# Performance work log

Measured on AMD Instinct MI355X. Metric: run time of the kernel, lower is better.

Reference implementation:

```python
import jax, jax.numpy as jnp
import numpy as np

NUM_FEATURE = 512
HIDDEN = 256
NUM_CLASSES = 10
L1 = 1e-4
ALPHA = 1e-3
BATCH = 65536


def setup_inputs() -> dict:
    key = jax.random.key(0)
    k = jax.random.split(key, 6)
    x = jax.random.normal(k[0], (BATCH, NUM_FEATURE), dtype=jnp.float32)
    y = jax.random.randint(k[1], (BATCH,), 0, NUM_CLASSES, dtype=jnp.int32)
    fc0 = jax.random.normal(k[2], (NUM_FEATURE, 512), dtype=jnp.float32) / NUM_FEATURE
    fc1 = jax.random.normal(k[3], (NUM_FEATURE, 512), dtype=jnp.float32) / NUM_FEATURE
    w = jax.random.normal(k[4], (NUM_FEATURE, HIDDEN), dtype=jnp.float32) / NUM_FEATURE
    w1 = jax.random.normal(k[5], (HIDDEN, NUM_CLASSES), dtype=jnp.float32) / HIDDEN
    return {"x": x, "y": y, "fc0": fc0, "fc1": fc1, "w": w, "w1": w1}


def reference(x, y, fc0, fc1, w, w1):
    # sigmoid-gated MLP block with residual
    x1 = x @ fc0                                   # [B, 512]
    x2 = jax.nn.relu(x @ fc1)                      # [B, 512]
    x4 = x + (1.0 + jax.nn.sigmoid(x1)) * x2       # [B, 512] residual

    # head (Dropout(p=0.0) is identity)
    logits = jax.nn.relu(x4 @ w) @ w1              # [B, 10]
    pred = jnp.argmax(logits, axis=1)

    # cross-entropy (mean over batch)
    logp = jax.nn.log_softmax(logits, axis=-1)
    ce = -jnp.mean(jnp.take_along_axis(logp, y[:, None].astype(jnp.int32), axis=1))

    # L1 penalty on all weight matrices
    l1_pen = L1 * (jnp.abs(w1).sum() + jnp.abs(w).sum()
                   + jnp.abs(fc0).sum() + jnp.abs(fc1).sum())

    # per-class variance: sum_i ||mean_{y_i} - x4_i||^2, vectorized via segment sums
    counts = jax.ops.segment_sum(jnp.ones((x4.shape[0],), jnp.float32), y,
                                 num_segments=NUM_CLASSES)
    sums = jax.ops.segment_sum(x4, y, num_segments=NUM_CLASSES)   # [10, 512]
    means = sums / jnp.maximum(counts, 1.0)[:, None]
    var_loss = jnp.sum(jnp.square(means[y] - x4))

    loss = ce + l1_pen + ALPHA * var_loss
    acc = jnp.mean((pred.astype(jnp.int32) == y.astype(jnp.int32)).astype(jnp.float32))
    return (loss, acc)
```

## Files before the change

kernel.cpp:

```cpp
#include <hip/hip_runtime.h>
#include <stdint.h>

#define BATCH 65536
#define FDIM 512
#define HDIM 256
#define NC 10
#define NREP 16

typedef short short8 __attribute__((ext_vector_type(8)));
typedef float f32x4 __attribute__((ext_vector_type(4)));

#define OFF_FC0T   ((size_t)0)
#define OFF_FC1T   (OFF_FC0T + (size_t)512*512*2)
#define OFF_WT     (OFF_FC1T + (size_t)512*512*2)
#define OFF_XT     (OFF_WT   + (size_t)256*512*2)
#define OFF_X4T    (OFF_XT   + (size_t)BATCH*512*2)
#define OFF_ACC    (OFF_X4T  + (size_t)BATCH*512*2)
#define SCAL_SUMSQ 0
#define SCAL_CE    16
#define SCAL_ACC   32
#define SCAL_L1    48
#define SCAL_N     128
#define CNT_OFF    SCAL_N
#define GSUM_OFF   (SCAL_N + NREP*16)
#define ACC_FLOATS (GSUM_OFF + NREP*5120)
#define OFF_W1T    (OFF_ACC + (size_t)ACC_FLOATS*4)

#define GLL(g,l) __builtin_amdgcn_global_load_lds((const __attribute__((address_space(1))) void*)(g), (__attribute__((address_space(3))) void*)(l), 16, 0, 0)

__device__ __forceinline__ unsigned short f2b(float f){
  unsigned u = __float_as_uint(f);
  u += 0x7FFFu + ((u >> 16) & 1u);
  return (unsigned short)(u >> 16);
}
__device__ __forceinline__ float b2f(unsigned short h){
  return __uint_as_float(((unsigned)h) << 16);
}
__device__ __forceinline__ unsigned pk2b(float f0, float f1){
  unsigned u0 = __float_as_uint(f0) + 0x8000u;
  unsigned u1 = __float_as_uint(f1) + 0x8000u;
  return __builtin_amdgcn_perm(u1, u0, 0x07060302u);
}

__global__ __launch_bounds__(256) void k_setup(
    const float* __restrict__ x,   const float* __restrict__ fc0,
    const float* __restrict__ fc1, const float* __restrict__ w,
    const float* __restrict__ w1,
    unsigned short* __restrict__ xT,   unsigned short* __restrict__ fc0T,
    unsigned short* __restrict__ fc1T, unsigned short* __restrict__ wT,
    unsigned short* __restrict__ w1T,  float* __restrict__ accb)
{
  int blk = blockIdx.x, t = threadIdx.x;
  if (blk < 1024){
    int I = blk*4 + (t >> 6);
    int l = t & 63;
    int row = I*16 + (l & 15), q = l >> 4;
    const float* src = x + (size_t)row*FDIM + q*8;
    #pragma unroll
    for (int C = 0; C < 16; ++C){
      float4 v0 = *(const float4*)(src + C*32);
      float4 v1 = *(const float4*)(src + C*32 + 4);
      unsigned o[4];
      o[0] = pk2b(v0.x, v0.y); o[1] = pk2b(v0.z, v0.w);
      o[2] = pk2b(v1.x, v1.y); o[3] = pk2b(v1.z, v1.w);
      *(short8*)&xT[(((size_t)I*16 + C) << 9) + l*8] = *(short8*)o;
    }
    return;
  }
  if (blk < 1360){
    int i = (blk - 1024)*256 + t;
    float l1v = 0.f;
    if (i < 32768){
      int n4 = i&15, m = (i>>4)&3, C = (i>>6)&15, J = i>>10;
      int n = J*16+n4, k8 = C*4+m;
      unsigned short o[8];
      #pragma unroll
      for (int j=0;j<8;++j){ float v = fc0[(size_t)(k8*8+j)*512 + n]; o[j]=f2b(v); l1v += fabsf(v); }
      *(short8*)&fc0T[(size_t)(J*16+C)*512 + (i&63)*8] = *(short8*)o;
    } else if (i < 65536){
      int j0 = i - 32768;
      int n4 = j0&15, m = (j0>>4)&3, C = (j0>>6)&15, J = j0>>10;
      int n = J*16+n4, k8 = C*4+m;
      unsigned short o[8];
      #pragma unroll
      for (int j=0;j<8;++j){ float v = fc1[(size_t)(k8*8+j)*512 + n]; o[j]=f2b(v); l1v += fabsf(v); }
      *(short8*)&fc1T[(size_t)(J*16+C)*512 + (j0&63)*8] = *(short8*)o;
    } else if (i < 81920){
      int j0 = i - 65536;
      int n4 = j0&15, m = (j0>>4)&3, C = (j0>>6)&15, J = j0>>10;
      int n = J*16+n4, k8 = C*4+m;
      unsigned short o[8];
      #pragma unroll
      for (int j=0;j<8;++j){ float v = w[(size_t)(k8*8+j)*256 + n]; o[j]=f2b(v); l1v += fabsf(v); }
      *(short8*)&wT[(size_t)(J*16+C)*512 + (j0&63)*8] = *(short8*)o;
    } else if (i < 86016){
      int j0 = i - 81920;
      int C = j0 >> 9, l = (j0 >> 3) & 63, e = j0 & 7;
      int n = l & 15, k = C*32 + (l>>4)*8 + e;
      float v = (n < NC) ? w1[k*NC + n] : 0.f;
      w1T[C*512 + l*8 + e] = f2b(v);
      if (n < NC) l1v = fabsf(v);
    }
    for (int off = 32; off; off >>= 1) l1v += __shfl_down(l1v, off);
    if ((t & 63) == 0 && l1v != 0.f)
      atomicAdd(&accb[SCAL_L1 + (blk & (NREP-1))], l1v);
    return;
  }
  {
    int base = (blk - 1360)*1024;
    #pragma unroll
    for (int j=0;j<4;++j){
      int idx = base + j*256 + t;
      if (idx < ACC_FLOATS) accb[idx] = 0.f;
    }
  }
}

__global__ __launch_bounds__(256) void k_gemm12(
    const unsigned short* __restrict__ xT,
    const unsigned short* __restrict__ fc0T,
    const unsigned short* __restrict__ fc1T,
    unsigned short* __restrict__ x4T,
    float* __restrict__ scal)
{
  __shared__ __align__(16) char lds[32768];
  unsigned short* As    = (unsigned short*)lds;
  unsigned short* Bs0   = (unsigned short*)(lds + 16384);
  unsigned short* Bs1   = (unsigned short*)(lds + 24576);
  unsigned short* trans = (unsigned short*)(lds + 16384);
  __shared__ float red[4];

  int blk = blockIdx.x;
  int xcd = blk & 7, s = blk >> 3;
  int rowblk = xcd*64 + (s >> 3);
  int colblk = s & 7;

  int t = threadIdx.x;
  int wv = t >> 6, lane = t & 63, ln = lane & 15, quad = lane >> 4;
  int wr = wv >> 1, wc = wv & 1;

  const f32x4 zv = {0.f,0.f,0.f,0.f};
  f32x4 acc1[4][2], acc2[4][2];
  #pragma unroll
  for (int rt=0;rt<4;++rt){ acc1[rt][0]=zv; acc1[rt][1]=zv; acc2[rt][0]=zv; acc2[rt][1]=zv; }

  const char* xb  = (const char*)xT;
  const char* b0b = (const char*)fc0T;
  const char* b1b = (const char*)fc1T;

  for (int kt = 0; kt < 8; ++kt){
    #pragma unroll
    for (int i = 0; i < 2; ++i)
      #pragma unroll
      for (int c = 0; c < 2; ++c){
        size_t Ig = (size_t)(rowblk*8 + wv*2 + i);
        GLL(xb + ((Ig*16 + kt*2 + c) << 10) + lane*16,
            (char*)As + (((wv*2+i)*2 + c) << 10));
      }
    {
      size_t Jg = (size_t)(colblk*4 + wv);
      const char* g0 = b0b + ((Jg*16 + kt*2) << 10) + lane*16;
      const char* g1 = b1b + ((Jg*16 + kt*2) << 10) + lane*16;
      GLL(g0,        (char*)Bs0 + ((wv*2+0) << 10));
      GLL(g0 + 1024, (char*)Bs0 + ((wv*2+1) << 10));
      GLL(g1,        (char*)Bs1 + ((wv*2+0) << 10));
      GLL(g1 + 1024, (char*)Bs1 + ((wv*2+1) << 10));
    }
    __syncthreads();
    #pragma unroll
    for (int c = 0; c < 2; ++c){
      short8 a[4];
      #pragma unroll
      for (int rt=0;rt<4;++rt)
        a[rt] = *(const short8*)&As[(((wr*4+rt)*2 + c) << 9) + lane*8];
      #pragma unroll
      for (int ct=0;ct<2;++ct){
        int jl = wc*2 + ct;
        short8 b0 = *(const short8*)&Bs0[((jl*2+c) << 9) + lane*8];
        #pragma unroll
        for (int rt=0;rt<4;++rt)
          acc1[rt][ct] = __builtin_amdgcn_mfma_f32_16x16x32_bf16(a[rt], b0, acc1[rt][ct], 0,0,0);
        short8 b1 = *(const short8*)&Bs1[((jl*2+c) << 9) + lane*8];
        #pragma unroll
        for (int rt=0;rt<4;++rt)
          acc2[rt][ct] = __builtin_amdgcn_mfma_f32_16x16x32_bf16(a[rt], b1, acc2[rt][ct], 0,0,0);
      }
    }
    __syncthreads();
  }

  #pragma unroll
  for (int i = 0; i < 2; ++i)
    #pragma unroll
    for (int c = 0; c < 2; ++c){
      size_t Ig = (size_t)(rowblk*8 + wv*2 + i);
      GLL(xb + ((Ig*16 + colblk*2 + c) << 10) + lane*16,
          (char*)As + (((wv*2+i)*2 + c) << 10));
    }
  __syncthreads();

  float sumsq = 0.f;
  #pragma unroll
  for (int rt=0;rt<4;++rt){
    #pragma unroll
    for (int ct=0;ct<2;++ct){
      int slot_hi = (ct*2 + (ln>>3)) << 4;
      int elem = ln & 7;
      #pragma unroll
      for (int r=0;r<4;++r){
        int addr = (((wr*4+rt)*2 + wc) << 9) + ((quad*4+r) | slot_hi)*8 + elem;
        float xv  = b2f(As[addr]);
        float x1v = acc1[rt][ct][r];
        float x2v = fmaxf(acc2[rt][ct][r], 0.f);
        float gate = 1.f + 1.f/(1.f + __expf(-x1v));
        float x4v = fmaf(gate, x2v, xv);
        unsigned short ub = f2b(x4v);
        float fq = b2f(ub);
        sumsq = fmaf(fq, fq, sumsq);
        trans[addr] = ub;
      }
    }
  }
  for (int off = 32; off; off >>= 1) sumsq += __shfl_down(sumsq, off);
  if (lane == 0) red[wv] = sumsq;
  __syncthreads();
  if (t == 0)
    atomicAdd(&scal[SCAL_SUMSQ + (blk & (NREP-1))], red[0]+red[1]+red[2]+red[3]);
  {
    int lt = t >> 4;
    int I_local = lt >> 1, C_local = lt & 1;
    size_t gbase = ((size_t)(rowblk*8 + I_local)*16 + colblk*2 + C_local) << 9;
    int s0 = (t & 15)*32;
    #pragma unroll
    for (int j=0;j<4;++j)
      *(short8*)&x4T[gbase + s0 + j*8] = *(const short8*)&trans[(lt << 9) + s0 + j*8];
  }
}

__global__ __launch_bounds__(256) void k_csum(const unsigned short* __restrict__ x4T,
                                              const int* __restrict__ y,
                                              float* __restrict__ gsum){
  int w = blockIdx.x*4 + (threadIdx.x >> 6);
  int l = threadIdx.x & 63;
  int C = w & 15, Ig = w >> 4;
  int rl = l & 15, q = l >> 4;
  float a[NC][8];
  #pragma unroll
  for (int c=0;c<NC;++c)
    #pragma unroll
    for (int e=0;e<8;++e) a[c][e]=0.f;
  for (int ii = 0; ii < 64; ++ii){
    int I = Ig*64 + ii;
    int yv = y[I*16 + rl];
    short8 v = *(const short8*)&x4T[(((size_t)I*16 + C) << 9) + l*8];
    float f[8];
    #pragma unroll
    for (int e=0;e<8;++e) f[e] = b2f((unsigned short)v[e]);
    #pragma unroll
    for (int c=0;c<NC;++c){
      bool m = (yv == c);
      #pragma unroll
      for (int e=0;e<8;++e) a[c][e] += m ? f[e] : 0.f;
    }
  }
  #pragma unroll
  for (int off = 1; off < 16; off <<= 1)
    #pragma unroll
    for (int c=0;c<NC;++c)
      #pragma unroll
      for (int e=0;e<8;++e) a[c][e] += __shfl_xor(a[c][e], off);
  if (rl == 0){
    int rep = Ig & (NREP-1);
    int kb = C*32 + q*8;
    #pragma unroll
    for (int c=0;c<NC;++c)
      #pragma unroll
      for (int e=0;e<8;++e)
        atomicAdd(&gsum[(size_t)rep*5120 + c*512 + kb + e], a[c][e]);
  }
}

__global__ __launch_bounds__(256) void k_cnt(const int* __restrict__ y,
                                             float* __restrict__ gcnt){
  __shared__ float cntS[NC];
  int t = threadIdx.x;
  if (t < NC) cntS[t] = 0.f;
  __syncthreads();
  int base = blockIdx.x*2048;
  for (int i = t; i < 2048; i += 256) atomicAdd(&cntS[y[base+i]], 1.f);
  __syncthreads();
  if (t < NC) atomicAdd(&gcnt[(blockIdx.x & (NREP-1))*16 + t], cntS[t]);
}

__global__ __launch_bounds__(512) void k_gemm3_head(
    const unsigned short* __restrict__ x4T,
    const unsigned short* __restrict__ wT,
    const unsigned short* __restrict__ w1T,
    const int* __restrict__ y,
    float* __restrict__ scal)
{
  __shared__ __align__(16) char lds[49152];
  unsigned short* As     = (unsigned short*)lds;
  unsigned short* Bs     = (unsigned short*)(lds + 16384);
  unsigned short* transH = (unsigned short*)lds;
  __shared__ __align__(16) unsigned short w1s[4096];
  __shared__ float redc[8], reda[8];

  int blk = blockIdx.x;
  int t = threadIdx.x;
  int wv = t >> 6, lane = t & 63, ln = lane & 15, quad = lane >> 4;
  int wr = wv >> 2, wc = wv & 3;
  int rep = (blk ^ (blk >> 4)) & (NREP-1);

  *(short8*)&w1s[t*8] = *(const short8*)&w1T[t*8];

  const f32x4 zv = {0.f,0.f,0.f,0.f};
  f32x4 acc[4][4];
  #pragma unroll
  for (int rt=0;rt<4;++rt)
    #pragma unroll
    for (int ct=0;ct<4;++ct) acc[rt][ct] = zv;

  const char* ab = (const char*)x4T;
  const char* bb = (const char*)wT;

  for (int kt = 0; kt < 8; ++kt){
    {
      size_t Ig = (size_t)(blk*8 + wv);
      GLL(ab + ((Ig*16 + kt*2 + 0) << 10) + lane*16, (char*)As + ((wv*2+0) << 10));
      GLL(ab + ((Ig*16 + kt*2 + 1) << 10) + lane*16, (char*)As + ((wv*2+1) << 10));
    }
    #pragma unroll
    for (int i = 0; i < 2; ++i)
      #pragma unroll
      for (int c = 0; c < 2; ++c){
        size_t Jg = (size_t)(wv*2 + i);
        GLL(bb + ((Jg*16 + kt*2 + c) << 10) + lane*16,
            (char*)Bs + (((wv*2+i)*2 + c) << 10));
      }
    __syncthreads();
    #pragma unroll
    for (int c = 0; c < 2; ++c){
      short8 a[4];
      #pragma unroll
      for (int rt=0;rt<4;++rt)
        a[rt] = *(const short8*)&As[(((wr*4+rt)*2 + c) << 9) + lane*8];
      #pragma unroll
      for (int ct=0;ct<4;++ct){
        short8 b = *(const short8*)&Bs[(((wc*4+ct)*2 + c) << 9) + lane*8];
        #pragma unroll
        for (int rt=0;rt<4;++rt)
          acc[rt][ct] = __builtin_amdgcn_mfma_f32_16x16x32_bf16(a[rt], b, acc[rt][ct], 0,0,0);
      }
    }
    __syncthreads();
  }

  f32x4 alog = zv;
  #pragma unroll
  for (int hf = 0; hf < 2; ++hf){
    __syncthreads();
    if ((wc >> 1) == hf){
      #pragma unroll
      for (int rt=0;rt<4;++rt)
        #pragma unroll
        for (int ct=0;ct<4;++ct)
          #pragma unroll
          for (int r=0;r<4;++r){
            int row_l = wr*64 + rt*16 + quad*4 + r;
            int ch = (wc & 1)*64 + ct*16 + ln;
            int tile = ((row_l >> 4) << 2) | (ch >> 5);
            int slot = (row_l & 15) | (((ch >> 3) & 3) << 4);
            transH[(tile << 9) + slot*8 + (ch & 7)] = f2b(fmaxf(acc[rt][ct][r], 0.f));
          }
    }
    __syncthreads();
    #pragma unroll
    for (int Cl = 0; Cl < 4; ++Cl){
      short8 a = *(const short8*)&transH[((wv*4 + Cl) << 9) + lane*8];
      short8 b = *(const short8*)&w1s[(hf*4 + Cl)*512 + lane*8];
      alog = __builtin_amdgcn_mfma_f32_16x16x32_bf16(a, b, alog, 0,0,0);
    }
  }

  float ce_l = 0.f, acc_l = 0.f;
  #pragma unroll
  for (int r = 0; r < 4; ++r){
    int grow = blk*128 + wv*16 + quad*4 + r;
    int yv = y[grow];
    float lg = (ln < NC) ? alog[r] : -1e30f;
    float m = lg; int mi = ln;
    #pragma unroll
    for (int mk = 1; mk < 16; mk <<= 1){
      float om = __shfl_xor(m, mk); int oi = __shfl_xor(mi, mk);
      if (om > m || (om == m && oi < mi)){ m = om; mi = oi; }
    }
    float e  = (ln < NC) ? __expf(lg - m) : 0.f;
    float sy = (ln == yv) ? lg : 0.f;
    #pragma unroll
    for (int mk = 1; mk < 16; mk <<= 1){ e += __shfl_xor(e, mk); sy += __shfl_xor(sy, mk); }
    float lse = m + __logf(e);
    if (ln == 0){ ce_l += (lse - sy); acc_l += (mi == yv) ? 1.f : 0.f; }
  }
  ce_l  += __shfl_down(ce_l, 16);  acc_l += __shfl_down(acc_l, 16);
  ce_l  += __shfl_down(ce_l, 32);  acc_l += __shfl_down(acc_l, 32);
  if (lane == 0){ redc[wv] = ce_l; reda[wv] = acc_l; }
  __syncthreads();
  if (t == 0){
    float c = 0.f, a = 0.f;
    #pragma unroll
    for (int i=0;i<8;++i){ c += redc[i]; a += reda[i]; }
    atomicAdd(&scal[SCAL_CE  + rep], c);
    atomicAdd(&scal[SCAL_ACC + rep], a);
  }
}

__global__ __launch_bounds__(1024) void k_final(const float* __restrict__ accb,
                                                float* __restrict__ out){
  const float* gsum = accb + GSUM_OFF;
  const float* gcnt = accb + CNT_OFF;
  int t = threadIdx.x;
  float contrib = 0.f;
  for (int idx = t; idx < 5120; idx += 1024){
    float S = 0.f;
    #pragma unroll
    for (int r = 0; r < NREP; ++r) S += gsum[(size_t)r*5120 + idx];
    int c = idx >> 9;
    float cnt = 0.f;
    #pragma unroll
    for (int r = 0; r < NREP; ++r) cnt += gcnt[r*16 + c];
    contrib += S*S / fmaxf(cnt, 1.f);
  }
  for (int off = 32; off; off >>= 1) contrib += __shfl_down(contrib, off);
  __shared__ float red[16];
  if ((t & 63) == 0) red[t >> 6] = contrib;
  __syncthreads();
  if (t == 0){
    float var2 = 0.f;
    #pragma unroll
    for (int i=0;i<16;++i) var2 += red[i];
    float sumsq=0.f, ce=0.f, acc=0.f, l1=0.f;
    for (int r=0;r<NREP;++r){
      sumsq += accb[SCAL_SUMSQ+r];
      ce    += accb[SCAL_CE+r];
      acc   += accb[SCAL_ACC+r];
      l1    += accb[SCAL_L1+r];
    }
    float var_loss = sumsq - var2;
    out[0] = ce/(float)BATCH + 1e-4f*l1 + 1e-3f*var_loss;
    out[1] = acc/(float)BATCH;
  }
}

extern "C" void kernel_launch(void* const* d_in, const int* in_sizes, int n_in,
                              void* d_out, int out_size, void* d_ws, size_t ws_size,
                              hipStream_t stream){
  (void)in_sizes; (void)n_in; (void)out_size; (void)ws_size;
  const float* x   = (const float*)d_in[0];
  const int*   y   = (const int*)d_in[1];
  const float* fc0 = (const float*)d_in[2];
  const float* fc1 = (const float*)d_in[3];
  const float* w   = (const float*)d_in[4];
  const float* w1  = (const float*)d_in[5];
  char* ws = (char*)d_ws;
  unsigned short* fc0T = (unsigned short*)(ws + OFF_FC0T);
  unsigned short* fc1T = (unsigned short*)(ws + OFF_FC1T);
  unsigned short* wT   = (unsigned short*)(ws + OFF_WT);
  unsigned short* xT   = (unsigned short*)(ws + OFF_XT);
  unsigned short* x4T  = (unsigned short*)(ws + OFF_X4T);
  unsigned short* w1T  = (unsigned short*)(ws + OFF_W1T);
  float* accb = (float*)(ws + OFF_ACC);
  float* scal = accb;
  float* gcnt = accb + CNT_OFF;
  float* gsum = accb + GSUM_OFF;

  k_setup<<<1441, 256, 0, stream>>>(x, fc0, fc1, w, w1, xT, fc0T, fc1T, wT, w1T, accb);
  k_gemm12<<<4096, 256, 0, stream>>>(xT, fc0T, fc1T, x4T, scal);
  k_cnt<<<32, 256, 0, stream>>>(y, gcnt);
  k_csum<<<256, 256, 0, stream>>>(x4T, y, gsum);
  k_gemm3_head<<<512, 512, 0, stream>>>(x4T, wT, w1T, y, scal);
  k_final<<<1, 1024, 0, stream>>>(accb, (float*)d_out);
}
```

Baseline: 410.1 us.

## Restructure gate GEMM into 256x128 tiles with double-buffered LDS pipeline

Rewrites the fused fc0/fc1 GEMM kernel to use 512-thread blocks computing 256-row by 128-column tiles, with 128 KB of dynamic LDS split into two buffers. Global-to-LDS loads for the next K steps are interleaved with MFMA phases under explicit barriers, vmcnt waits and raised priority around the MFMA phases. Larger tiles cut redundant reloads of x and the weights, and the prefetching is meant to hide load latency behind compute. The cost is more registers per thread and heavy LDS use, which limits how many blocks fit on each CU.

Result: no change. 404.5 us (-1.4%).

```diff
diff --git a/kernel.cpp b/kernel.cpp
--- a/kernel.cpp
+++ b/kernel.cpp
@@ -116,124 +116,172 @@
   }
 }
 
-__global__ __launch_bounds__(256) void k_gemm12(
+
+#define BARRIER() __builtin_amdgcn_s_barrier()
+#define LGKM0() do{ asm volatile("s_waitcnt lgkmcnt(0)" ::: "memory"); \
+                    __builtin_amdgcn_sched_barrier(0); }while(0)
+
+#define READA(A, AB, H) do{                                                   \
+  _Pragma("unroll") for (int c_=0;c_<2;++c_)                                  \
+  _Pragma("unroll") for (int m_=0;m_<4;++m_)                                  \
+    A[c_][m_] = *(const short8*)((AB) + (((wr*8 + (H)*4 + m_)*2 + c_)<<10) + lane*16); \
+}while(0)
+
+#define READB(B, BB, MAT) do{                                                 \
+  _Pragma("unroll") for (int c_=0;c_<2;++c_)                                  \
+  _Pragma("unroll") for (int n_=0;n_<2;++n_)                                  \
+    B[c_][n_] = *(const short8*)((BB) + (MAT)*16384 + (((wc*2+n_)*2 + c_)<<10) + lane*16); \
+}while(0)
+
+#define MM(ACC, MB, A, B) do{                                                 \
+  __builtin_amdgcn_s_setprio(1);                                              \
+  _Pragma("unroll") for (int c_=0;c_<2;++c_)                                  \
+  _Pragma("unroll") for (int n_=0;n_<2;++n_)                                  \
+  _Pragma("unroll") for (int m_=0;m_<4;++m_)                                  \
+    ACC[(MB)+m_][n_] = __builtin_amdgcn_mfma_f32_16x16x32_bf16(A[c_][m_], B[c_][n_], ACC[(MB)+m_][n_], 0,0,0); \
+  __builtin_amdgcn_s_setprio(0);                                              \
+}while(0)
+
+#define STAGEA(KT2, H) do{                                                    \
+  char* d_ = ldsd + (((KT2)&1) ? 65536 : 0);                                  \
+  _Pragma("unroll") for (int r_=0;r_<2;++r_){                                 \
+    int idx_ = r_*8 + wv, q_ = idx_>>1, C_ = idx_&1;                          \
+    int Il_ = (q_&3) + ((q_>>2)<<3) + (H)*4;                                  \
+    GLL(xb + (((size_t)((rowblk*16 + Il_)*16 + (KT2)*2 + C_)) << 10) + lane*16, \
+        d_ + ((Il_*2 + C_) << 10) + lane*16);                                 \
+  } }while(0)
+
+#define STAGEB(KT2, MAT) do{                                                  \
+  char* d_ = ldsd + (((KT2)&1) ? 65536 : 0) + 32768 + (MAT)*16384;            \
+  const char* s_ = (MAT) ? b1b : b0b;                                         \
+  _Pragma("unroll") for (int r_=0;r_<2;++r_){                                 \
+    int idx_ = r_*8 + wv, J_ = idx_>>1, C_ = idx_&1;                          \
+    GLL(s_ + (((size_t)((colblk*8 + J_)*16 + (KT2)*2 + C_)) << 10) + lane*16, \
+        d_ + ((J_*2 + C_) << 10) + lane*16);                                  \
+  } }while(0)
+
+__global__ __launch_bounds__(512, 2) void k_gemm12(
     const unsigned short* __restrict__ xT,
     const unsigned short* __restrict__ fc0T,
     const unsigned short* __restrict__ fc1T,
     unsigned short* __restrict__ x4T,
     float* __restrict__ scal)
 {
-  __shared__ __align__(16) char lds[32768];
-  unsigned short* As    = (unsigned short*)lds;
-  unsigned short* Bs0   = (unsigned short*)(lds + 16384);
-  unsigned short* Bs1   = (unsigned short*)(lds + 24576);
-  unsigned short* trans = (unsigned short*)(lds + 16384);
-  __shared__ float red[4];
+  extern __shared__ __align__(16) char ldsd[];
 
   int blk = blockIdx.x;
-  int xcd = blk & 7, s = blk >> 3;
-  int rowblk = xcd*64 + (s >> 3);
-  int colblk = s & 7;
+  int wg = (blk & 7)*128 + (blk >> 3);
+  int rowblk = wg >> 2;
+  int colblk = wg & 3;
 
   int t = threadIdx.x;
   int wv = t >> 6, lane = t & 63, ln = lane & 15, quad = lane >> 4;
-  int wr = wv >> 1, wc = wv & 1;
-
-  const f32x4 zv = {0.f,0.f,0.f,0.f};
-  f32x4 acc1[4][2], acc2[4][2];
-  #pragma unroll
-  for (int rt=0;rt<4;++rt){ acc1[rt][0]=zv; acc1[rt][1]=zv; acc2[rt][0]=zv; acc2[rt][1]=zv; }
+  int wr = wv >> 2, wc = wv & 3;
 
   const char* xb  = (const char*)xT;
   const char* b0b = (const char*)fc0T;
   const char* b1b = (const char*)fc1T;
 
+  const f32x4 zv = {0.f,0.f,0.f,0.f};
+  f32x4 acc1[8][2], acc2[8][2];
+  #pragma unroll
+  for (int m=0;m<8;++m){ acc1[m][0]=zv; acc1[m][1]=zv; acc2[m][0]=zv; acc2[m][1]=zv; }
+
+  STAGEA(0,0); STAGEA(0,1); STAGEB(0,0); STAGEB(0,1);
+  STAGEB(1,0); STAGEA(1,1);
+  asm volatile("s_waitcnt vmcnt(4)" ::: "memory");
+  __builtin_amdgcn_sched_barrier(0);
+  BARRIER();
+
+  short8 a0[2][4], a1[2][4], bb[2][2];
+
   for (int kt = 0; kt < 8; ++kt){
-    #pragma unroll
-    for (int i = 0; i < 2; ++i)
-      #pragma unroll
-      for (int c = 0; c < 2; ++c){
-        size_t Ig = (size_t)(rowblk*8 + wv*2 + i);
-        GLL(xb + ((Ig*16 + kt*2 + c) << 10) + lane*16,
-            (char*)As + (((wv*2+i)*2 + c) << 10));
-      }
-    {
-      size_t Jg = (size_t)(colblk*4 + wv);
-      const char* g0 = b0b + ((Jg*16 + kt*2) << 10) + lane*16;
-      const char* g1 = b1b + ((Jg*16 + kt*2) << 10) + lane*16;
-      GLL(g0,        (char*)Bs0 + ((wv*2+0) << 10));
-      GLL(g0 + 1024, (char*)Bs0 + ((wv*2+1) << 10));
-      GLL(g1,        (char*)Bs1 + ((wv*2+0) << 10));
-      GLL(g1 + 1024, (char*)Bs1 + ((wv*2+1) << 10));
-    }
-    __syncthreads();
-    #pragma unroll
-    for (int c = 0; c < 2; ++c){
-      short8 a[4];
-      #pragma unroll
-      for (int rt=0;rt<4;++rt)
-        a[rt] = *(const short8*)&As[(((wr*4+rt)*2 + c) << 9) + lane*8];
-      #pragma unroll
-      for (int ct=0;ct<2;++ct){
-        int jl = wc*2 + ct;
-        short8 b0 = *(const short8*)&Bs0[((jl*2+c) << 9) + lane*8];
-        #pragma unroll
-        for (int rt=0;rt<4;++rt)
-          acc1[rt][ct] = __builtin_amdgcn_mfma_f32_16x16x32_bf16(a[rt], b0, acc1[rt][ct], 0,0,0);
-        short8 b1 = *(const short8*)&Bs1[((jl*2+c) << 9) + lane*8];
-        #pragma unroll
-        for (int rt=0;rt<4;++rt)
-          acc2[rt][ct] = __builtin_amdgcn_mfma_f32_16x16x32_bf16(a[rt], b1, acc2[rt][ct], 0,0,0);
-      }
-    }
-    __syncthreads();
-  }
-
-  #pragma unroll
-  for (int i = 0; i < 2; ++i)
-    #pragma unroll
-    for (int c = 0; c < 2; ++c){
-      size_t Ig = (size_t)(rowblk*8 + wv*2 + i);
-      GLL(xb + ((Ig*16 + colblk*2 + c) << 10) + lane*16,
-          (char*)As + (((wv*2+i)*2 + c) << 10));
-    }
-  __syncthreads();
-
+    char* Ab = ldsd + ((kt&1) ? 65536 : 0);
+    char* Bb = Ab + 32768;
+
+    READA(a0, Ab, 0);
+    READB(bb, Bb, 0);
+    if (kt < 7) STAGEA(kt+1, 0);
+    BARRIER(); LGKM0();
+    MM(acc1, 0, a0, bb);
+    BARRIER();
+
+    READA(a1, Ab, 1);
+    if (kt < 7) STAGEB(kt+1, 1);
+    BARRIER(); LGKM0();
+    MM(acc1, 4, a1, bb);
+    BARRIER();
+
+    READB(bb, Bb, 1);
+    if (kt < 6) STAGEB(kt+2, 0);
+    BARRIER(); LGKM0();
+    MM(acc2, 4, a1, bb);
+    BARRIER();
+
+    READA(a0, Ab, 0);
+    if (kt < 6) STAGEA(kt+2, 1);
+    BARRIER(); LGKM0();
+    MM(acc2, 0, a0, bb);
+    if (kt < 6)       { asm volatile("s_waitcnt vmcnt(4)" ::: "memory"); }
+    else if (kt == 6) { asm volatile("s_waitcnt vmcnt(0)" ::: "memory"); }
+    __builtin_amdgcn_sched_barrier(0);
+    BARRIER();
+  }
+
+  {
+    int Cres = colblk*4 + wc;
+    #pragma unroll
+    for (int i = 0; i < 8; ++i){
+      GLL(xb + (((size_t)((rowblk*16 + wr*8 + i)*16 + Cres)) << 10) + lane*16,
+          ldsd + ((wv*8 + i) << 10) + lane*16);
+    }
+    asm volatile("s_waitcnt vmcnt(0)" ::: "memory");
+  }
+  __syncthreads();
+
+  unsigned short* resU = (unsigned short*)ldsd;
+  unsigned short* x4U  = (unsigned short*)(ldsd + 65536);
   float sumsq = 0.f;
   #pragma unroll
-  for (int rt=0;rt<4;++rt){
-    #pragma unroll
-    for (int ct=0;ct<2;++ct){
-      int slot_hi = (ct*2 + (ln>>3)) << 4;
-      int elem = ln & 7;
-      #pragma unroll
-      for (int r=0;r<4;++r){
-        int addr = (((wr*4+rt)*2 + wc) << 9) + ((quad*4+r) | slot_hi)*8 + elem;
-        float xv  = b2f(As[addr]);
-        float x1v = acc1[rt][ct][r];
-        float x2v = fmaxf(acc2[rt][ct][r], 0.f);
+  for (int m = 0; m < 8; ++m){
+    #pragma unroll
+    for (int n = 0; n < 2; ++n){
+      #pragma unroll
+      for (int r = 0; r < 4; ++r){
+        int slot = (quad*4 + r) | ((n*2 + (ln>>3)) << 4);
+        int idx = ((wv*8 + m) << 9) + slot*8 + (ln & 7);
+        float xv  = b2f(resU[idx]);
+        float x1v = acc1[m][n][r];
+        float x2v = fmaxf(acc2[m][n][r], 0.f);
         float gate = 1.f + 1.f/(1.f + __expf(-x1v));
         float x4v = fmaf(gate, x2v, xv);
         unsigned short ub = f2b(x4v);
         float fq = b2f(ub);
         sumsq = fmaf(fq, fq, sumsq);
-        trans[addr] = ub;
+        x4U[idx] = ub;
       }
     }
   }
   for (int off = 32; off; off >>= 1) sumsq += __shfl_down(sumsq, off);
+  __syncthreads();
+  float* red = (float*)ldsd;
   if (lane == 0) red[wv] = sumsq;
   __syncthreads();
-  if (t == 0)
-    atomicAdd(&scal[SCAL_SUMSQ + (blk & (NREP-1))], red[0]+red[1]+red[2]+red[3]);
-  {
-    int lt = t >> 4;
-    int I_local = lt >> 1, C_local = lt & 1;
-    size_t gbase = ((size_t)(rowblk*8 + I_local)*16 + colblk*2 + C_local) << 9;
-    int s0 = (t & 15)*32;
-    #pragma unroll
-    for (int j=0;j<4;++j)
-      *(short8*)&x4T[gbase + s0 + j*8] = *(const short8*)&trans[(lt << 9) + s0 + j*8];
+  if (t == 0){
+    float s = 0.f;
+    #pragma unroll
+    for (int i=0;i<8;++i) s += red[i];
+    atomicAdd(&scal[SCAL_SUMSQ + (blk & (NREP-1))], s);
+  }
+  #pragma unroll
+  for (int r = 0; r < 2; ++r){
+    int o = r*512 + t;
+    int tile = o >> 6, off16 = o & 63;
+    int wvp = tile >> 3, i = tile & 7;
+    size_t Ig = (size_t)rowblk*16 + (wvp>>2)*8 + i;
+    int Cg = colblk*4 + (wvp & 3);
+    *(short8*)&x4T[((Ig*16 + Cg) << 9) + off16*8] =
+      *(const short8*)&x4U[(tile << 9) + off16*8];
   }
 }
 
@@ -474,8 +522,15 @@
   float* gcnt = accb + CNT_OFF;
   float* gsum = accb + GSUM_OFF;
 
+  static bool once = [](){
+    hipFuncSetAttribute((const void*)k_gemm12,
+                        hipFuncAttributeMaxDynamicSharedMemorySize, 131072);
+    return true;
+  }();
+  (void)once;
+
   k_setup<<<1441, 256, 0, stream>>>(x, fc0, fc1, w, w1, xT, fc0T, fc1T, wT, w1T, accb);
-  k_gemm12<<<4096, 256, 0, stream>>>(xT, fc0T, fc1T, x4T, scal);
+  k_gemm12<<<1024, 512, 131072, stream>>>(xT, fc0T, fc1T, x4T, scal);
   k_cnt<<<32, 256, 0, stream>>>(y, gcnt);
   k_csum<<<256, 256, 0, stream>>>(x4T, y, gsum);
   k_gemm3_head<<<512, 512, 0, stream>>>(x4T, wT, w1T, y, scal);
```
